# Kernel optimization log

Measured on AMD Instinct MI355X. Metric: run time of the kernel, lower is better.

## Reference

```python
import jax, jax.numpy as jnp
import numpy as np

PAD, BOS = 0, 1
EPS = 1e-08


def _lstm_cell(xt, h, c, wih, whh, bih, bhh):
    z = xt @ wih.T + h @ whh.T + bih + bhh
    i, f, g, o = jnp.split(z, 4, axis=-1)  # torch gate order i,f,g,o
    c = jax.nn.sigmoid(f) * c + jax.nn.sigmoid(i) * jnp.tanh(g)
    h = jax.nn.sigmoid(o) * jnp.tanh(c)
    return h, c


def _run_lstm(emb, wih, whh, bih, bhh):
    B, H = emb.shape[0], whh.shape[1]
    def step(carry, xt):
        h, c = _lstm_cell(xt, carry[0], carry[1], wih, whh, bih, bhh)
        return (h, c), h
    init = (jnp.zeros((B, H), emb.dtype), jnp.zeros((B, H), emb.dtype))
    (hT, cT), outs = jax.lax.scan(step, init, jnp.swapaxes(emb, 0, 1))
    return jnp.swapaxes(outs, 0, 1), hT, cT


def setup_inputs() -> dict:
    key = jax.random.key(0)
    V, H, B, S, T = 32000, 256, 8, 200, 51
    ks = jax.random.split(key, 24)
    def n(i, shape, s=0.02):
        return jax.random.normal(ks[i], shape, jnp.float32) * s
    x = jax.random.randint(ks[0], (B, S), 1, V)
    x = x.at[:, -1].set(V - 1)  # pins extended vocab size to 2V
    labels = jax.random.randint(ks[1], (B, T), 1, V)
    return {
        "x": x, "labels": labels, "ext_vocab_size": 2 * V,
        "emb_enc": n(2, (V, H)).at[PAD].set(0.0),
        "wih_f": n(3, (4 * H, H)), "whh_f": n(4, (4 * H, H)),
        "bih_f": jnp.zeros((4 * H,), jnp.float32), "bhh_f": jnp.zeros((4 * H,), jnp.float32),
        "wih_b": n(5, (4 * H, H)), "whh_b": n(6, (4 * H, H)),
        "bih_b": jnp.zeros((4 * H,), jnp.float32), "bhh_b": jnp.zeros((4 * H,), jnp.float32),
        "w_sel1": n(7, (H, 2 * H)), "b_sel1": jnp.zeros((H,), jnp.float32),
        "w_sel2": n(8, (1, H)), "b_sel2": jnp.zeros((1,), jnp.float32),
        "w_rh": n(9, (H, 2 * H)), "b_rh": jnp.zeros((H,), jnp.float32),
        "w_rc": n(10, (H, 2 * H)), "b_rc": jnp.zeros((H,), jnp.float32),
        "emb_dec": n(11, (V, H)).at[PAD].set(0.0),
        "wih_d": n(12, (4 * H, 3 * H)), "whh_d": n(13, (4 * H, H)),
        "bih_d": jnp.zeros((4 * H,), jnp.float32), "bhh_d": jnp.zeros((4 * H,), jnp.float32),
        "w_attn": n(14, (H, 4 * H)), "b_attn": jnp.zeros((H,), jnp.float32),
        "w_attn_v": n(15, (1, H)),
        "w_ptr": n(16, (1, 3 * H)), "b_ptr": jnp.zeros((1,), jnp.float32),
        "w_gen": n(17, (V, H)), "b_gen": jnp.zeros((V,), jnp.float32),
        "w_cov": n(18, (H, 1)), "b_cov": jnp.zeros((H,), jnp.float32),
    }


def reference(x, labels, ext_vocab_size, emb_enc, wih_f, whh_f, bih_f, bhh_f,
              wih_b, whh_b, bih_b, bhh_b, w_sel1, b_sel1, w_sel2, b_sel2,
              w_rh, b_rh, w_rc, b_rc, emb_dec, wih_d, whh_d, bih_d, bhh_d,
              w_attn, b_attn, w_attn_v, w_ptr, b_ptr, w_gen, b_gen, w_cov, b_cov):
    B, S = x.shape
    V, H = w_gen.shape
    # ---- Encoder: BiLSTM (no padding -> packing is identity; eval -> no dropout)
    emb = emb_enc[x]  # [B,S,H]
    out_f, h_f, c_f = _run_lstm(emb, wih_f, whh_f, bih_f, bhh_f)
    out_b_r, h_b, c_b = _run_lstm(emb[:, ::-1], wih_b, whh_b, bih_b, bhh_b)
    enc_out = jnp.concatenate([out_f, out_b_r[:, ::-1]], axis=-1)  # [B,S,2H]
    copy_probs = jax.nn.sigmoid(
        (jnp.tanh(enc_out @ w_sel1.T + b_sel1) @ w_sel2.T + b_sel2)[..., 0])  # [B,S]
    # ---- bidirectional state reduction
    h0 = jax.nn.relu(jnp.concatenate([h_f, h_b], -1) @ w_rh.T + b_rh)
    c0 = jax.nn.relu(jnp.concatenate([c_f, c_b], -1) @ w_rc.T + b_rc)
    # ---- Decoder loop (teacher forcing): inputs = [BOS, labels[:,1:T-1]]
    dec_in = jnp.concatenate(
        [jnp.full((B, 1), BOS, labels.dtype), labels[:, 1:-1]], axis=1)  # [B,T-1]
    mask_cp = (copy_probs > EPS).astype(jnp.float32)
    rows = jnp.arange(B)[:, None]

    def step(carry, tok):
        h, c, cov = carry
        cov_feat = cov[..., None] * w_cov[:, 0] + b_cov  # [B,S,H]
        feats = jnp.concatenate(
            [enc_out, jnp.broadcast_to(h[:, None, :], (B, S, H)), cov_feat], axis=-1)
        e = jnp.tanh(feats @ w_attn.T + b_attn)           # [B,S,H]
        attn = jax.nn.softmax(e @ w_attn_v[0], axis=1)    # [B,S]
        attn = attn * mask_cp
        attn = attn / (attn.sum(1, keepdims=True) + 1e-10)
        cov = cov + attn
        ctx = jnp.einsum('bs,bsd->bd', attn, enc_out)     # [B,2H]
        h, c = _lstm_cell(jnp.concatenate([emb_dec[tok], ctx], -1), h, c,
                          wih_d, whh_d, bih_d, bhh_d)
        p_gen = jax.nn.sigmoid(jnp.concatenate([ctx, h], -1) @ w_ptr.T + b_ptr)  # [B,1]
        vocab_dist = jax.nn.softmax(h @ w_gen.T + b_gen, axis=-1)  # [B,V]
        dist = jnp.zeros((B, ext_vocab_size), jnp.float32)
        dist = dist.at[:, :V].set(p_gen * vocab_dist)
        dist = dist.at[rows, x].add((1.0 - p_gen) * attn)  # pointer/copy scatter-add
        return (h, c, cov), dist

    cov0 = jnp.zeros((B, S), jnp.float32)
    _, outs = jax.lax.scan(step, (h0, c0, cov0), dec_in.T)
    outputs = jnp.swapaxes(outs, 0, 1)  # [B,T-1,EV]
    # ---- loss (faithful: CE treats the mixture distribution as logits)
    targets = labels[:, 1:]
    logp = jax.nn.log_softmax(outputs, axis=-1)
    nll = -jnp.take_along_axis(logp, targets[..., None], axis=-1)[..., 0]
    valid = (targets != PAD).astype(jnp.float32)
    loss_ce = (nll * valid).sum() / valid.sum()
    m = (x != PAD).astype(jnp.float32)
    lp = jnp.clip(jnp.log(copy_probs), -100.0, None)
    l1p = jnp.clip(jnp.log1p(-copy_probs), -100.0, None)
    bce = -(m * lp + (1.0 - m) * l1p)
    loss = loss_ce + 1.0 * (bce * m).sum() / m.sum()
    return outputs, loss
```

## Files before the change

### kernel.cpp

```cpp
#include <hip/hip_runtime.h>
#include <hip/hip_bf16.h>
#include <stdint.h>


#define DEVI __device__ __forceinline__
#define AT_RLX __ATOMIC_RELAXED
#define SC_AGT __HIP_MEMORY_SCOPE_AGENT

static constexpr size_t OFF_ACC   = 0;
static constexpr size_t OFF_FLAGE = 4;
static constexpr size_t OFF_FLAGD = 36;
static constexpr size_t ZERO_FLOATS = 200;
static constexpr size_t OFF_CTX   = 256;
static constexpr size_t OFF_EMB   = 4352;
static constexpr size_t OFF_HSEL  = OFF_EMB;
static constexpr size_t OFF_HP    = OFF_EMB;
static constexpr size_t OFF_PREF  = OFF_EMB  + 409600;
static constexpr size_t OFF_PREB  = OFF_PREF + 1638400;
static constexpr size_t OFF_BIAS  = OFF_PREB + 1638400;
static constexpr size_t OFF_HB    = OFF_BIAS + 3072;
static constexpr size_t OFF_HFIN  = OFF_HB   + 8192;
static constexpr size_t OFF_CFIN  = OFF_HFIN + 4096;
static constexpr size_t OFF_ENCOUT= OFF_CFIN + 4096;
static constexpr size_t OFF_MASK  = OFF_ENCOUT + 819200;
static constexpr size_t OFF_C0    = OFF_MASK + 1600;
static constexpr size_t OFF_EP    = OFF_C0   + 2048;
static constexpr size_t OFF_WCP   = OFF_EP   + 409600;
static constexpr size_t OFF_BCP   = OFF_WCP  + 256;
static constexpr size_t OFF_DEMB  = OFF_BCP  + 256;
static constexpr size_t OFF_DPRE  = OFF_DEMB + 102400;
static constexpr size_t OFF_HBUF  = OFF_DPRE + 409600;
static constexpr size_t OFF_CS    = OFF_HBUF + 4096;
static constexpr size_t OFF_HS    = OFF_CS   + 204800;
static constexpr size_t OFF_AS    = OFF_HS   + 102400;
static constexpr size_t OFF_PG    = OFF_AS   + 80000;
static constexpr size_t OFF_PE    = OFF_PG   + 512;

DEVI float sigf(float x)      { return 1.0f / (1.0f + __expf(-x)); }
DEVI float tanh_fast(float x) { return 1.0f - 2.0f / (1.0f + __expf(2.0f * x)); }
DEVI float ald(const float* p)  { return __hip_atomic_load((float*)p, AT_RLX, SC_AGT); }
DEVI void  ast(float* p, float v){ __hip_atomic_store(p, v, AT_RLX, SC_AGT); }

DEVI void fbar(int* flags, int g, int n, int val) {
  __syncthreads();
  if ((int)threadIdx.x == 0)
    __hip_atomic_store(flags + g, val, AT_RLX, SC_AGT);
  if ((int)threadIdx.x < n && (int)threadIdx.x != g) {
    while (__hip_atomic_load(flags + threadIdx.x, AT_RLX, SC_AGT) < val)
      __builtin_amdgcn_s_sleep(1);
  }
  __syncthreads();
}

__global__ __launch_bounds__(256) void k_biassum(
    const float* bih_f, const float* bhh_f, const float* bih_b, const float* bhh_b,
    const float* bih_d, const float* bhh_d, float* ws) {
  int i = blockIdx.x * 256 + threadIdx.x;
  int which = i >> 10, jj = i & 1023;
  float v = (which == 0) ? bih_f[jj] + bhh_f[jj]
          : (which == 1) ? bih_b[jj] + bhh_b[jj]
                         : bih_d[jj] + bhh_d[jj];
  ws[OFF_BIAS + i] = v;
}

__global__ __launch_bounds__(256) void k_embed(
    const int* xin, const int* labels, const float* emb_enc, const float* emb_dec, float* ws) {
  int r = blockIdx.x, h = threadIdx.x;
  if (r < 1600) {
    int t = r >> 3, b = r & 7;
    ws[OFF_EMB + (size_t)r * 256 + h] = emb_enc[(size_t)xin[b * 200 + t] * 256 + h];
  } else {
    int r2 = r - 1600;
    int t = r2 >> 3, b = r2 & 7;
    int tok = (t == 0) ? 1 : labels[b * 51 + t];
    ws[OFF_DEMB + (size_t)r2 * 256 + h] = emb_dec[(size_t)tok * 256 + h];
  }
}

template<int BM, int BN, int TM, int TN, int CMAP, int ACT, int AMAP>
__global__ __launch_bounds__(256) void k_gemm(
    const float* __restrict__ A, const float* __restrict__ B,
    const float* __restrict__ bias, float* __restrict__ C,
    int M, int K, int ldb, int ldc) {
  __shared__ float As[16][BM];
  __shared__ float Bs[16][BN];
  const int tid = threadIdx.x;
  const int tx = tid & 15, ty = tid >> 4;
  const int m0 = blockIdx.x * BM, n0 = blockIdx.y * BN;
  float acc[TM][TN];
#pragma unroll
  for (int i = 0; i < TM; ++i)
#pragma unroll
    for (int q = 0; q < TN; ++q) acc[i][q] = 0.f;

  for (int kk = 0; kk < K; kk += 16) {
#pragma unroll
    for (int e = tid; e < BM * 4; e += 256) {
      int m = e >> 2, k4 = (e & 3) * 4;
      int gm0 = m0 + m;
      float4 v = {0.f, 0.f, 0.f, 0.f};
      if (gm0 < M) {
        int gm = AMAP ? (((199 - (gm0 >> 3)) << 3) + (gm0 & 7)) : gm0;
        v = *(const float4*)(A + (size_t)gm * K + kk + k4);
      }
      As[k4 + 0][m] = v.x; As[k4 + 1][m] = v.y; As[k4 + 2][m] = v.z; As[k4 + 3][m] = v.w;
    }
#pragma unroll
    for (int e = tid; e < BN * 4; e += 256) {
      int n = e >> 2, k4 = (e & 3) * 4;
      float4 v = *(const float4*)(B + (size_t)(n0 + n) * ldb + kk + k4);
      Bs[k4 + 0][n] = v.x; Bs[k4 + 1][n] = v.y; Bs[k4 + 2][n] = v.z; Bs[k4 + 3][n] = v.w;
    }
    __syncthreads();
#pragma unroll
    for (int k = 0; k < 16; ++k) {
      float a[TM], bv[TN];
#pragma unroll
      for (int i = 0; i < TM; ++i) a[i] = As[k][ty * TM + i];
#pragma unroll
      for (int q = 0; q < TN; ++q) bv[q] = Bs[k][tx * TN + q];
#pragma unroll
      for (int i = 0; i < TM; ++i)
#pragma unroll
        for (int q = 0; q < TN; ++q) acc[i][q] += a[i] * bv[q];
    }
    __syncthreads();
  }
#pragma unroll
  for (int i = 0; i < TM; ++i) {
    int gm = m0 + ty * TM + i;
    if (gm >= M) continue;
    size_t base;
    if (CMAP == 1) { int t = gm >> 3, b = gm & 7; base = (size_t)(b * 50 + t) * 64000; }
    else            base = (size_t)gm * ldc;
#pragma unroll
    for (int q = 0; q < TN; ++q) {
      int n = n0 + tx * TN + q;
      float v = acc[i][q] + bias[n];
      if (ACT == 1) v = tanh_fast(v);
      C[base + n] = v;
    }
  }
}

__global__ __launch_bounds__(512, 1) void k_encoder(
    const float* __restrict__ whh_f, const float* __restrict__ whh_b, float* __restrict__ ws) {
  __shared__ float hs2[2048];
  __shared__ float zs[512];
  const int dir = blockIdx.x >> 4;
  const int p   = blockIdx.x & 15;
  const int u0  = p * 16;
  const float* whh = dir ? whh_b : whh_f;
  const float* pre = ws + (dir ? OFF_PREB : OFF_PREF);
  unsigned long long* hp = (unsigned long long*)(ws + OFF_HP);
  const int tid = threadIdx.x;
  const int kc4 = tid & 15;
  const int jp  = tid >> 4;
  const int jj0 = jp * 2, jj1 = jj0 + 1;
  const int jg0 = (jj0 >> 4) * 256 + u0 + (jj0 & 15);
  const int jg1 = (jj1 >> 4) * 256 + u0 + (jj1 & 15);
  float4 W0[4], W1[4];
  {
    const float* w0 = whh + (size_t)jg0 * 256 + kc4 * 16;
    const float* w1 = whh + (size_t)jg1 * 256 + kc4 * 16;
#pragma unroll
    for (int q = 0; q < 4; ++q) { W0[q] = *(const float4*)(w0 + q * 4);
                                  W1[q] = *(const float4*)(w1 + q * 4); }
  }
  const int jlf = kc4 >> 3, bf = kc4 & 7;
  const int jjf = jp * 2 + jlf;
  const int jf  = (jjf >> 4) * 256 + u0 + (jjf & 15);
  const int zsl = (jjf >> 4) * 128 + (jjf & 15) * 8 + bf;
  const int wb_ = tid >> 6;
  const int kk0 = (tid * 4) & 255;
  const int wdst = wb_ * 256 + ((kk0 >> 2) & 3) * 64 + (kk0 >> 4) * 4;
  const int ui2 = tid & 15, b2 = tid >> 4;
  float c_reg = 0.f;
  float* enc = ws + OFF_ENCOUT;

  for (int t = 0; t < 200; ++t) {
    float pre_v = pre[((size_t)t * 8 + bf) * 1024 + jf];
    float acc[16];
#pragma unroll
    for (int i = 0; i < 16; ++i) acc[i] = 0.f;
    if (t > 0) {
      unsigned long long* src = hp + (size_t)((((t + 1) & 1) * 2 + dir) * 2048) + tid * 4;
      const unsigned long long e = (unsigned long long)(unsigned)t;
      unsigned long long a0, a1, a2, a3;
      for (;;) {
        a0 = __hip_atomic_load(src + 0, AT_RLX, SC_AGT);
        a1 = __hip_atomic_load(src + 1, AT_RLX, SC_AGT);
        a2 = __hip_atomic_load(src + 2, AT_RLX, SC_AGT);
        a3 = __hip_atomic_load(src + 3, AT_RLX, SC_AGT);
        if (((a0 >> 32) == e) && ((a1 >> 32) == e) &&
            ((a2 >> 32) == e) && ((a3 >> 32) == e)) break;
        __builtin_amdgcn_s_sleep(1);
      }
      float4 hv;
      hv.x = __uint_as_float((unsigned)a0);
      hv.y = __uint_as_float((unsigned)a1);
      hv.z = __uint_as_float((unsigned)a2);
      hv.w = __uint_as_float((unsigned)a3);
      *(float4*)(&hs2[wdst]) = hv;
    }
    __syncthreads();
    if (t > 0) {
#pragma unroll
      for (int b = 0; b < 8; ++b) {
        const float* hb = &hs2[b * 256 + kc4 * 4];
#pragma unroll
        for (int q = 0; q < 4; ++q) {
          float4 h4 = *(const float4*)(hb + q * 64);
          acc[b]     = fmaf(W0[q].x, h4.x, acc[b]);
          acc[b]     = fmaf(W0[q].y, h4.y, acc[b]);
          acc[b]     = fmaf(W0[q].z, h4.z, acc[b]);
          acc[b]     = fmaf(W0[q].w, h4.w, acc[b]);
          acc[8 + b] = fmaf(W1[q].x, h4.x, acc[8 + b]);
          acc[8 + b] = fmaf(W1[q].y, h4.y, acc[8 + b]);
          acc[8 + b] = fmaf(W1[q].z, h4.z, acc[8 + b]);
          acc[8 + b] = fmaf(W1[q].w, h4.w, acc[8 + b]);
        }
      }
    }
    {
      bool h8 = (kc4 & 8) != 0;
#pragma unroll
      for (int i = 0; i < 8; ++i) {
        float send = h8 ? acc[i] : acc[i + 8];
        float keep = h8 ? acc[i + 8] : acc[i];
        acc[i] = keep + __shfl_xor(send, 8);
      }
      bool h4b = (kc4 & 4) != 0;
#pragma unroll
      for (int i = 0; i < 4; ++i) {
        float send = h4b ? acc[i] : acc[i + 4];
        float keep = h4b ? acc[i + 4] : acc[i];
        acc[i] = keep + __shfl_xor(send, 4);
      }
      bool h2b = (kc4 & 2) != 0;
#pragma unroll
      for (int i = 0; i < 2; ++i) {
        float send = h2b ? acc[i] : acc[i + 2];
        float keep = h2b ? acc[i + 2] : acc[i];
        acc[i] = keep + __shfl_xor(send, 2);
      }
      bool h1b = (kc4 & 1) != 0;
      {
        float send = h1b ? acc[0] : acc[1];
        float keep = h1b ? acc[1] : acc[0];
        acc[0] = keep + __shfl_xor(send, 1);
      }
    }
    zs[zsl] = acc[0] + pre_v;
    __syncthreads();
    if (tid < 128) {
      int i0 = ui2 * 8 + b2;
      float zi = zs[i0], zf = zs[128 + i0], zg = zs[256 + i0], zo = zs[384 + i0];
      float cn = sigf(zf) * c_reg + sigf(zi) * tanh_fast(zg);
      float hn = sigf(zo) * tanh_fast(cn);
      c_reg = cn;
      int uu = u0 + ui2;
      if (t < 199) {
        unsigned long long pk =
            ((unsigned long long)(unsigned)(t + 1) << 32) |
            (unsigned long long)__float_as_uint(hn);
        __hip_atomic_store(hp + (size_t)(((t & 1) * 2 + dir) * 2048) + b2 * 256 + uu,
                           pk, AT_RLX, SC_AGT);
      }
      int s = dir ? (199 - t) : t;
      enc[((size_t)b2 * 200 + s) * 512 + dir * 256 + uu] = hn;
      if (t == 199) {
        ws[OFF_HFIN + (size_t)(dir * 8 + b2) * 256 + uu] = hn;
        ws[OFF_CFIN + (size_t)(dir * 8 + b2) * 256 + uu] = cn;
      }
    }
  }
}

__global__ __launch_bounds__(64) void k_selbce(
    const float* w_sel2, const float* b_sel2, const int* xin, float* ws) {
  int r = blockIdx.x, lane = threadIdx.x;
  float pacc = 0.f;
#pragma unroll
  for (int i = 0; i < 4; ++i) {
    int k = lane + 64 * i;
    pacc += ws[OFF_HSEL + (size_t)r * 256 + k] * w_sel2[k];
  }
#pragma unroll
  for (int m = 1; m < 64; m <<= 1) pacc += __shfl_xor(pacc, m);
  if (lane == 0) {
    float cp = sigf(pacc + b_sel2[0]);
    ws[OFF_MASK + r] = (cp > 1e-8f) ? 1.f : 0.f;
    int b = r / 200, s = r % 200;
    float m = (xin[b * 200 + s] != 0) ? 1.f : 0.f;
    if (m > 0.f) {
      float lp = fmaxf(logf(cp), -100.f);
      atomicAdd(ws + OFF_ACC + 2, -lp);
    }
    atomicAdd(ws + OFF_ACC + 3, m);
  }
}

__global__ __launch_bounds__(256) void k_wcp(
    const float* w_attn, const float* w_cov, const float* b_cov, float* ws) {
  int jj = threadIdx.x;
  float a = 0.f, c = 0.f;
  for (int h = 0; h < 256; ++h) {
    float w = w_attn[(size_t)jj * 1024 + 768 + h];
    a += w * w_cov[h];
    c += w * b_cov[h];
  }
  ws[OFF_WCP + jj] = a;
  ws[OFF_BCP + jj] = c;
}

__global__ __launch_bounds__(256) void k_h0c0(
    const float* w_rh, const float* b_rh, const float* w_rc, const float* b_rc, float* ws) {
  int b = blockIdx.x, jj = threadIdx.x;
  const float* hf  = ws + OFF_HFIN + (size_t)b * 256;
  const float* hbk = ws + OFF_HFIN + 2048 + (size_t)b * 256;
  const float* cf  = ws + OFF_CFIN + (size_t)b * 256;
  const float* cbk = ws + OFF_CFIN + 2048 + (size_t)b * 256;
  float ah = b_rh[jj], ac = b_rc[jj];
  for (int k = 0; k < 256; ++k) {
    ah += hf[k] * w_rh[(size_t)jj * 512 + k];
    ac += cf[k] * w_rc[(size_t)jj * 512 + k];
  }
  for (int k = 0; k < 256; ++k) {
    ah += hbk[k] * w_rh[(size_t)jj * 512 + 256 + k];
    ac += cbk[k] * w_rc[(size_t)jj * 512 + 256 + k];
  }
  ws[OFF_C0 + (size_t)b * 256 + jj] = fmaxf(ac, 0.f);
  ws[OFF_HBUF + (size_t)b * 256 + jj] = fmaxf(ah, 0.f);
}

__global__ __launch_bounds__(512, 1) void k_decoder(
    const float* __restrict__ wih_d, const float* __restrict__ whh_d,
    const float* __restrict__ w_attn, const float* __restrict__ w_attn_v,
    float* __restrict__ ws) {
  __shared__ float hc_s[8 * 768];
  __shared__ float h_pad[264];
  __shared__ float hw_q[64];
  __shared__ float e_s[256];
  __shared__ float at_s[256], cv_s[256], msk_s[256];
  __shared__ float zs_l[256];
  __shared__ float wcq_s[64], bcq_s[64], wvq_s[64];
  __shared__ float mS_s[2];
  const int g = blockIdx.x, tid = threadIdx.x;
  const int b1 = g >> 2, sq = g & 3, s0 = sq * 50;
  int* flags = (int*)(ws + OFF_FLAGD);
  const int jl = tid >> 3, kq = tid & 7;
  const int kseg = tid & 15, row_l = tid >> 4;
  const int u_l = row_l & 7, gate = row_l >> 3;
  const int j = gate * 256 + g * 8 + u_l;
  float4 W48[12];
#pragma unroll
  for (int q = 0; q < 12; ++q) {
    int k0 = 4 * kseg + 64 * q;
    W48[q] = (k0 < 512) ? *(const float4*)(wih_d + (size_t)j * 768 + 256 + k0)
                        : *(const float4*)(whh_d + (size_t)j * 256 + (k0 - 512));
  }
  float4 W32[8];
  {
    const float* wsrc = w_attn + (size_t)(sq * 64 + jl) * 1024 + 512 + kq * 32;
#pragma unroll
    for (int q = 0; q < 8; ++q) W32[q] = *(const float4*)(wsrc + q * 4);
  }
  const int u_c = tid & 7, b_c = tid >> 3;
  float c_reg = (tid < 64) ? ws[OFF_C0 + (size_t)b_c * 256 + g * 8 + u_c] : 0.f;
  for (int s = tid; s < 256; s += 512) {
    msk_s[s] = (s < 200) ? ws[OFF_MASK + b1 * 200 + s] : 0.f;
    cv_s[s] = 0.f;
  }
  if (tid < 64) {
    wcq_s[tid] = ws[OFF_WCP + sq * 64 + tid];
    bcq_s[tid] = ws[OFF_BCP + sq * 64 + tid];
    wvq_s[tid] = w_attn_v[sq * 64 + tid];
  }
  __syncthreads();

  for (int t = 0; t < 50; ++t) {
    const int rb = t & 1, wb = 1 - rb;
    if (tid < 128) ast(ws + OFF_CTX + g * 128 + tid, 0.f);
    if (tid < 256) {
      float v = ald(ws + OFF_HBUF + (size_t)rb * 2048 + b1 * 256 + tid);
      h_pad[(tid >> 5) * 33 + (tid & 31)] = v;
    }
    __syncthreads();
    {
      float a = 0.f;
      const float* hq = &h_pad[kq * 33];
#pragma unroll
      for (int q = 0; q < 8; ++q) {
        float4 h4 = { hq[q * 4 + 0], hq[q * 4 + 1], hq[q * 4 + 2], hq[q * 4 + 3] };
        a = fmaf(W32[q].x, h4.x, a);
        a = fmaf(W32[q].y, h4.y, a);
        a = fmaf(W32[q].z, h4.z, a);
        a = fmaf(W32[q].w, h4.w, a);
      }
      a += __shfl_xor(a, 1);
      a += __shfl_xor(a, 2);
      a += __shfl_xor(a, 4);
      if (kq == 0) hw_q[jl] = a;
    }
    __syncthreads();
    if (tid < 200) {
      const int s = tid;
      float cv = cv_s[s];
      const float* ep = ws + OFF_EP + ((size_t)(b1 * 200 + s)) * 256 + sq * 64;
      float pe = 0.f;
#pragma unroll
      for (int i4 = 0; i4 < 16; ++i4) {
        float4 e4 = *(const float4*)(ep + i4 * 4);
        float4 h4 = *(const float4*)(&hw_q[i4 * 4]);
        float4 w4 = *(const float4*)(&wcq_s[i4 * 4]);
        float4 b4 = *(const float4*)(&bcq_s[i4 * 4]);
        float4 v4 = *(const float4*)(&wvq_s[i4 * 4]);
        pe = fmaf(tanh_fast(e4.x + h4.x + cv * w4.x + b4.x), v4.x, pe);
        pe = fmaf(tanh_fast(e4.y + h4.y + cv * w4.y + b4.y), v4.y, pe);
        pe = fmaf(tanh_fast(e4.z + h4.z + cv * w4.z + b4.z), v4.z, pe);
        pe = fmaf(tanh_fast(e4.w + h4.w + cv * w4.w + b4.w), v4.w, pe);
      }
      ast(ws + OFF_PE + (size_t)(sq * 8 + b1) * 200 + s, pe);
    }
    fbar(flags, g, 32, 3 * t + 1);

    if (tid < 200) {
      float e0 = ald(ws + OFF_PE + (size_t)(0 * 8 + b1) * 200 + tid);
      float e1 = ald(ws + OFF_PE + (size_t)(1 * 8 + b1) * 200 + tid);
      float e2 = ald(ws + OFF_PE + (size_t)(2 * 8 + b1) * 200 + tid);
      float e3 = ald(ws + OFF_PE + (size_t)(3 * 8 + b1) * 200 + tid);
      e_s[tid] = (e0 + e1) + (e2 + e3);
    }
    __syncthreads();
    if (tid < 64) {
      float m = -1e30f;
#pragma unroll
      for (int i = 0; i < 4; ++i) {
        int s = tid + 64 * i;
        if (s < 200) m = fmaxf(m, e_s[s]);
      }
#pragma unroll
      for (int md = 1; md < 64; md <<= 1) m = fmaxf(m, __shfl_xor(m, md));
      float es = 0.f, ems = 0.f;
#pragma unroll
      for (int i = 0; i < 4; ++i) {
        int s = tid + 64 * i;
        if (s < 200) {
          float e = __expf(e_s[s] - m);
          es += e; ems += e * msk_s[s];
        }
      }
#pragma unroll
      for (int md = 1; md < 64; md <<= 1) { es += __shfl_xor(es, md); ems += __shfl_xor(ems, md); }
      if (tid == 0) { mS_s[0] = m; mS_s[1] = 1.0f / (ems + 1e-10f * es); }
    }
    __syncthreads();
    if (tid < 200) {
      float a = __expf(e_s[tid] - mS_s[0]) * msk_s[tid] * mS_s[1];
      at_s[tid] = a;
      cv_s[tid] += a;
      if (tid >= s0 && tid < s0 + 50)
        ws[OFF_AS + ((size_t)t * 8 + b1) * 200 + tid] = a;
    }
    __syncthreads();
    {
      float ca = 0.f;
      const float* ebase = ws + OFF_ENCOUT + ((size_t)(b1 * 200 + s0)) * 512 + tid;
#pragma unroll 10
      for (int s2 = 0; s2 < 50; ++s2)
        ca = fmaf(at_s[s0 + s2], ebase[(size_t)s2 * 512], ca);
      atomicAdd(ws + OFF_CTX + b1 * 512 + tid, ca);
    }
    fbar(flags, g, 32, 3 * t + 2);

    for (int e = tid; e < 6144; e += 512) {
      int bb = e / 768, kk2 = e % 768;
      hc_s[e] = (kk2 < 512) ? ald(ws + OFF_CTX + bb * 512 + kk2)
                            : ald(ws + OFF_HBUF + (size_t)rb * 2048 + bb * 256 + (kk2 - 512));
    }
    __syncthreads();
    if (g < 8) ws[OFF_CS + ((size_t)t * 8 + g) * 512 + tid] = hc_s[g * 768 + tid];
    float acc[8];
#pragma unroll
    for (int b = 0; b < 8; ++b) acc[b] = 0.f;
#pragma unroll
    for (int q = 0; q < 12; ++q) {
      int k0 = 4 * kseg + 64 * q;
#pragma unroll
      for (int b = 0; b < 8; ++b) {
        float4 h4 = *(const float4*)(&hc_s[b * 768 + k0]);
        acc[b] = fmaf(W48[q].x, h4.x, acc[b]);
        acc[b] = fmaf(W48[q].y, h4.y, acc[b]);
        acc[b] = fmaf(W48[q].z, h4.z, acc[b]);
        acc[b] = fmaf(W48[q].w, h4.w, acc[b]);
      }
    }
    {
      bool h8 = (kseg & 8) != 0;
#pragma unroll
      for (int i = 0; i < 4; ++i) {
        float send = h8 ? acc[i] : acc[i + 4];
        float keep = h8 ? acc[i + 4] : acc[i];
        acc[i] = keep + __shfl_xor(send, 8);
      }
      bool h4b = (kseg & 4) != 0;
#pragma unroll
      for (int i = 0; i < 2; ++i) {
        float send = h4b ? acc[i] : acc[i + 2];
        float keep = h4b ? acc[i + 2] : acc[i];
        acc[i] = keep + __shfl_xor(send, 4);
      }
      bool h2b = (kseg & 2) != 0;
      {
        float send = h2b ? acc[0] : acc[1];
        float keep = h2b ? acc[1] : acc[0];
        acc[0] = keep + __shfl_xor(send, 2);
      }
      acc[0] += __shfl_xor(acc[0], 1);
    }
    {
      int bz = kseg >> 1;
      float z = acc[0] + ws[OFF_DPRE + ((size_t)t * 8 + bz) * 1024 + j];
      if ((kseg & 1) == 0) zs_l[row_l * 8 + bz] = z;
    }
    __syncthreads();
    if (tid < 64) {
      float zi = zs_l[(0  + u_c) * 8 + b_c];
      float zf = zs_l[(8  + u_c) * 8 + b_c];
      float zg = zs_l[(16 + u_c) * 8 + b_c];
      float zo = zs_l[(24 + u_c) * 8 + b_c];
      float cn = sigf(zf) * c_reg + sigf(zi) * tanh_fast(zg);
      float hn = sigf(zo) * tanh_fast(cn);
      c_reg = cn;
      ast(ws + OFF_HBUF + (size_t)wb * 2048 + b_c * 256 + g * 8 + u_c, hn);
      ws[OFF_HS + ((size_t)t * 8 + b_c) * 256 + g * 8 + u_c] = hn;
    }
    fbar(flags, g, 32, 3 * t + 3);
  }
}

__global__ __launch_bounds__(64) void k_pgen(const float* w_ptr, const float* b_ptr, float* ws) {
  int r = blockIdx.x, lane = threadIdx.x;
  float p = 0.f;
#pragma unroll
  for (int i = 0; i < 12; ++i) {
    int k = lane + 64 * i;
    float v = (k < 512) ? ws[OFF_CS + (size_t)r * 512 + k]
                        : ws[OFF_HS + (size_t)r * 256 + (k - 512)];
    p += v * w_ptr[k];
  }
#pragma unroll
  for (int m = 1; m < 64; m <<= 1) p += __shfl_xor(p, m);
  if (lane == 0) ws[OFF_PG + r] = sigf(p + b_ptr[0]);
}

__global__ __launch_bounds__(256) void k_v2(const int* xin, const int* labels, float* ws, float* out) {
  __shared__ float redm[256], reds[256];
  __shared__ int xv[200];
  __shared__ float s1sh, corrsh;
  int r = blockIdx.x, tid = threadIdx.x;
  int tt = r >> 3, b = r & 7;
  float* row = out + (size_t)(b * 50 + tt) * 64000;
  for (int i = tid; i < 200; i += 256) xv[i] = xin[b * 200 + i];
  float m = -1e30f, s = 0.f;
  for (int i = tid; i < 32000; i += 256) {
    float z = row[i];
    float nm = fmaxf(m, z);
    s = s * __expf(m - nm) + __expf(z - nm);
    m = nm;
  }
  redm[tid] = m; reds[tid] = s;
  __syncthreads();
  for (int st = 128; st >= 1; st >>= 1) {
    if (tid < st) {
      float m2 = redm[tid + st], s2 = reds[tid + st];
      float M = fmaxf(redm[tid], m2);
      reds[tid] = reds[tid] * __expf(redm[tid] - M) + s2 * __expf(m2 - M);
      redm[tid] = M;
    }
    __syncthreads();
  }
  float mx = redm[0], sum = reds[0];
  float pg = ws[OFF_PG + r];
  __syncthreads();
  float s1 = 0.f;
  float inv = 1.0f / sum;
  for (int i = tid; i < 32000; i += 256) {
    float z = row[i];
    float d = pg * (__expf(z - mx) * inv);
    row[i] = d;
    s1 += __expf(d);
  }
  for (int i = 32000 + tid; i < 64000; i += 256) row[i] = 0.0f;
  reds[tid] = s1;
  __syncthreads();
  for (int st = 128; st >= 1; st >>= 1) { if (tid < st) reds[tid] += reds[tid + st]; __syncthreads(); }
  if (tid == 0) { s1sh = reds[0]; corrsh = 0.f; }
  __syncthreads();
  if (tid < 200) {
    int v = xv[tid];
    bool own = true;
    for (int s2 = 0; s2 < tid; ++s2) if (xv[s2] == v) { own = false; break; }
    if (own) {
      float delta = 0.f;
      for (int s2 = tid; s2 < 200; ++s2)
        if (xv[s2] == v) delta += ws[OFF_AS + (size_t)r * 200 + s2];
      delta *= (1.0f - pg);
      float base = row[v];
      row[v] = base + delta;
      atomicAdd(&corrsh, __expf(base + delta) - __expf(base));
    }
  }
  __syncthreads();
  if (tid == 0) {
    float lse = logf(s1sh + corrsh + 32000.0f);
    int tgt = labels[b * 51 + tt + 1];
    float dt = row[tgt];
    float valid = (tgt != 0) ? 1.f : 0.f;
    atomicAdd(ws + OFF_ACC + 0, valid * (lse - dt));
    atomicAdd(ws + OFF_ACC + 1, valid);
  }
}

__global__ void k_loss(float* ws, float* out, int out_size) {
  out[out_size - 1] = ws[OFF_ACC + 0] / ws[OFF_ACC + 1] + ws[OFF_ACC + 2] / ws[OFF_ACC + 3];
}

extern "C" void kernel_launch(void* const* d_in, const int* in_sizes, int n_in,
                              void* d_out, int out_size, void* d_ws, size_t ws_size,
                              hipStream_t stream) {
  (void)in_sizes; (void)n_in; (void)ws_size;
  const int*   x       = (const int*)  d_in[0];
  const int*   labels  = (const int*)  d_in[1];
  const float* emb_enc = (const float*)d_in[3];
  const float* wih_f   = (const float*)d_in[4];
  const float* whh_f   = (const float*)d_in[5];
  const float* bih_f   = (const float*)d_in[6];
  const float* bhh_f   = (const float*)d_in[7];
  const float* wih_b   = (const float*)d_in[8];
  const float* whh_b   = (const float*)d_in[9];
  const float* bih_b   = (const float*)d_in[10];
  const float* bhh_b   = (const float*)d_in[11];
  const float* w_sel1  = (const float*)d_in[12];
  const float* b_sel1  = (const float*)d_in[13];
  const float* w_sel2  = (const float*)d_in[14];
  const float* b_sel2  = (const float*)d_in[15];
  const float* w_rh    = (const float*)d_in[16];
  const float* b_rh    = (const float*)d_in[17];
  const float* w_rc    = (const float*)d_in[18];
  const float* b_rc    = (const float*)d_in[19];
  const float* emb_dec = (const float*)d_in[20];
  const float* wih_d   = (const float*)d_in[21];
  const float* whh_d   = (const float*)d_in[22];
  const float* bih_d   = (const float*)d_in[23];
  const float* bhh_d   = (const float*)d_in[24];
  const float* w_attn  = (const float*)d_in[25];
  const float* b_attn  = (const float*)d_in[26];
  const float* w_attn_v= (const float*)d_in[27];
  const float* w_ptr   = (const float*)d_in[28];
  const float* b_ptr   = (const float*)d_in[29];
  const float* w_gen   = (const float*)d_in[30];
  const float* b_gen   = (const float*)d_in[31];
  const float* w_cov   = (const float*)d_in[32];
  const float* b_cov   = (const float*)d_in[33];
  float* ws  = (float*)d_ws;
  float* out = (float*)d_out;

  hipMemsetAsync(d_ws, 0, ZERO_FLOATS * 4, stream);
  k_biassum<<<12, 256, 0, stream>>>(bih_f, bhh_f, bih_b, bhh_b, bih_d, bhh_d, ws);
  k_embed<<<2000, 256, 0, stream>>>(x, labels, emb_enc, emb_dec, ws);
  k_gemm<64,64,4,4,0,0,0><<<dim3(25,16), 256, 0, stream>>>(ws+OFF_EMB,  wih_f, ws+OFF_BIAS,      ws+OFF_PREF, 1600, 256, 256, 1024);
  k_gemm<64,64,4,4,0,0,1><<<dim3(25,16), 256, 0, stream>>>(ws+OFF_EMB,  wih_b, ws+OFF_BIAS+1024, ws+OFF_PREB, 1600, 256, 256, 1024);
  k_gemm<64,64,4,4,0,0,0><<<dim3(7,16),  256, 0, stream>>>(ws+OFF_DEMB, wih_d, ws+OFF_BIAS+2048, ws+OFF_DPRE, 400,  256, 768, 1024);
  hipMemsetAsync((void*)(ws + OFF_HP), 0, (size_t)2 * 2 * 2048 * sizeof(unsigned long long), stream);
  k_encoder<<<32, 512, 0, stream>>>(whh_f, whh_b, ws);
  k_gemm<64,64,4,4,0,1,0><<<dim3(25,4),  256, 0, stream>>>(ws+OFF_ENCOUT, w_sel1, b_sel1, ws+OFF_HSEL, 1600, 512, 512, 256);
  k_selbce<<<1600, 64, 0, stream>>>(w_sel2, b_sel2, x, ws);
  k_gemm<64,64,4,4,0,0,0><<<dim3(25,4),  256, 0, stream>>>(ws+OFF_ENCOUT, w_attn, b_attn, ws+OFF_EP, 1600, 512, 1024, 256);
  k_wcp<<<1, 256, 0, stream>>>(w_attn, w_cov, b_cov, ws);
  k_h0c0<<<8, 256, 0, stream>>>(w_rh, b_rh, w_rc, b_rc, ws);
  k_decoder<<<32, 512, 0, stream>>>(wih_d, whh_d, w_attn, w_attn_v, ws);
  k_pgen<<<400, 64, 0, stream>>>(w_ptr, b_ptr, ws);
  k_gemm<128,128,8,8,1,0,0><<<dim3(4,250), 256, 0, stream>>>(ws+OFF_HS, w_gen, b_gen, out, 400, 256, 256, 64000);
  k_v2<<<400, 256, 0, stream>>>(x, labels, ws, out);
  k_loss<<<1, 1, 0, stream>>>(ws, out, out_size);
}
```

Baseline: 2.073 ms.

## Replace decoder flag barriers with step-tagged dataflow exchanges

Removes the three per-step global flag barriers in the persistent decoder kernel. Hidden state, partial attention energies and partial context vectors now travel as 64-bit words that pack the step number with the value, and consumers spin until their tag matches. The context atomicAdd becomes four per-quarter partials summed by the reader. This lets blocks proceed as soon as their own inputs are ready instead of waiting on all 32 blocks, at the cost of more polling loads, double-width traffic and an extra memset to clear the tags.

```diff
diff --git a/kernel.cpp b/kernel.cpp
--- a/kernel.cpp
+++ b/kernel.cpp
@@ -15,6 +15,10 @@
 static constexpr size_t OFF_EMB   = 4352;
 static constexpr size_t OFF_HSEL  = OFF_EMB;
 static constexpr size_t OFF_HP    = OFF_EMB;
+static constexpr size_t OFF_DHP   = OFF_EMB;
+static constexpr size_t OFF_DPE   = OFF_EMB + 8192;
+static constexpr size_t OFF_DCX   = OFF_EMB + 20992;
+static constexpr size_t DTAG_FLOATS = 53760;
 static constexpr size_t OFF_PREF  = OFF_EMB  + 409600;
 static constexpr size_t OFF_PREB  = OFF_PREF + 1638400;
 static constexpr size_t OFF_BIAS  = OFF_PREB + 1638400;
@@ -40,16 +44,11 @@
 DEVI float tanh_fast(float x) { return 1.0f - 2.0f / (1.0f + __expf(2.0f * x)); }
 DEVI float ald(const float* p)  { return __hip_atomic_load((float*)p, AT_RLX, SC_AGT); }
 DEVI void  ast(float* p, float v){ __hip_atomic_store(p, v, AT_RLX, SC_AGT); }
-
-DEVI void fbar(int* flags, int g, int n, int val) {
-  __syncthreads();
-  if ((int)threadIdx.x == 0)
-    __hip_atomic_store(flags + g, val, AT_RLX, SC_AGT);
-  if ((int)threadIdx.x < n && (int)threadIdx.x != g) {
-    while (__hip_atomic_load(flags + threadIdx.x, AT_RLX, SC_AGT) < val)
-      __builtin_amdgcn_s_sleep(1);
-  }
-  __syncthreads();
+DEVI unsigned long long aldu(const unsigned long long* p) {
+  return __hip_atomic_load((unsigned long long*)p, AT_RLX, SC_AGT);
+}
+DEVI void astu(unsigned long long* p, unsigned long long v) {
+  __hip_atomic_store(p, v, AT_RLX, SC_AGT);
 }
 
 __global__ __launch_bounds__(256) void k_biassum(
@@ -188,10 +187,7 @@
       const unsigned long long e = (unsigned long long)(unsigned)t;
       unsigned long long a0, a1, a2, a3;
       for (;;) {
-        a0 = __hip_atomic_load(src + 0, AT_RLX, SC_AGT);
-        a1 = __hip_atomic_load(src + 1, AT_RLX, SC_AGT);
-        a2 = __hip_atomic_load(src + 2, AT_RLX, SC_AGT);
-        a3 = __hip_atomic_load(src + 3, AT_RLX, SC_AGT);
+        a0 = aldu(src + 0); a1 = aldu(src + 1); a2 = aldu(src + 2); a3 = aldu(src + 3);
         if (((a0 >> 32) == e) && ((a1 >> 32) == e) &&
             ((a2 >> 32) == e) && ((a3 >> 32) == e)) break;
         __builtin_amdgcn_s_sleep(1);
@@ -264,8 +260,7 @@
         unsigned long long pk =
             ((unsigned long long)(unsigned)(t + 1) << 32) |
             (unsigned long long)__float_as_uint(hn);
-        __hip_atomic_store(hp + (size_t)(((t & 1) * 2 + dir) * 2048) + b2 * 256 + uu,
-                           pk, AT_RLX, SC_AGT);
+        astu(hp + (size_t)(((t & 1) * 2 + dir) * 2048) + b2 * 256 + uu, pk);
       }
       int s = dir ? (199 - t) : t;
       enc[((size_t)b2 * 200 + s) * 512 + dir * 256 + uu] = hn;
@@ -331,7 +326,8 @@
     ac += cbk[k] * w_rc[(size_t)jj * 512 + 256 + k];
   }
   ws[OFF_C0 + (size_t)b * 256 + jj] = fmaxf(ac, 0.f);
-  ws[OFF_HBUF + (size_t)b * 256 + jj] = fmaxf(ah, 0.f);
+  unsigned long long* hp2 = (unsigned long long*)(ws + OFF_DHP);
+  hp2[(size_t)b * 256 + jj] = (unsigned long long)__float_as_uint(fmaxf(ah, 0.f));
 }
 
 __global__ __launch_bounds__(512, 1) void k_decoder(
@@ -348,7 +344,9 @@
   __shared__ float mS_s[2];
   const int g = blockIdx.x, tid = threadIdx.x;
   const int b1 = g >> 2, sq = g & 3, s0 = sq * 50;
-  int* flags = (int*)(ws + OFF_FLAGD);
+  unsigned long long* hp2 = (unsigned long long*)(ws + OFF_DHP);
+  unsigned long long* pe2 = (unsigned long long*)(ws + OFF_DPE);
+  unsigned long long* cx2 = (unsigned long long*)(ws + OFF_DCX);
   const int jl = tid >> 3, kq = tid & 7;
   const int kseg = tid & 15, row_l = tid >> 4;
   const int u_l = row_l & 7, gate = row_l >> 3;
@@ -381,10 +379,17 @@
 
   for (int t = 0; t < 50; ++t) {
     const int rb = t & 1, wb = 1 - rb;
-    if (tid < 128) ast(ws + OFF_CTX + g * 128 + tid, 0.f);
+    const unsigned long long tgH = (unsigned long long)(unsigned)t;
+    const unsigned long long tgP = (unsigned long long)(unsigned)(t + 1);
     if (tid < 256) {
-      float v = ald(ws + OFF_HBUF + (size_t)rb * 2048 + b1 * 256 + tid);
-      h_pad[(tid >> 5) * 33 + (tid & 31)] = v;
+      unsigned long long* src = hp2 + (size_t)rb * 2048 + b1 * 256 + tid;
+      unsigned long long v;
+      for (;;) {
+        v = aldu(src);
+        if ((v >> 32) == tgH) break;
+        __builtin_amdgcn_s_sleep(1);
+      }
+      h_pad[(tid >> 5) * 33 + (tid & 31)] = __uint_as_float((unsigned)v);
     }
     __syncthreads();
     {
@@ -421,16 +426,24 @@
         pe = fmaf(tanh_fast(e4.z + h4.z + cv * w4.z + b4.z), v4.z, pe);
         pe = fmaf(tanh_fast(e4.w + h4.w + cv * w4.w + b4.w), v4.w, pe);
       }
-      ast(ws + OFF_PE + (size_t)(sq * 8 + b1) * 200 + s, pe);
-    }
-    fbar(flags, g, 32, 3 * t + 1);
+      astu(pe2 + (size_t)(sq * 8 + b1) * 200 + s,
+           (tgP << 32) | (unsigned long long)__float_as_uint(pe));
+    }
 
     if (tid < 200) {
-      float e0 = ald(ws + OFF_PE + (size_t)(0 * 8 + b1) * 200 + tid);
-      float e1 = ald(ws + OFF_PE + (size_t)(1 * 8 + b1) * 200 + tid);
-      float e2 = ald(ws + OFF_PE + (size_t)(2 * 8 + b1) * 200 + tid);
-      float e3 = ald(ws + OFF_PE + (size_t)(3 * 8 + b1) * 200 + tid);
-      e_s[tid] = (e0 + e1) + (e2 + e3);
+      float esum = 0.f;
+#pragma unroll
+      for (int q = 0; q < 4; ++q) {
+        unsigned long long* src = pe2 + (size_t)(q * 8 + b1) * 200 + tid;
+        unsigned long long v;
+        for (;;) {
+          v = aldu(src);
+          if ((v >> 32) == tgP) break;
+          __builtin_amdgcn_s_sleep(1);
+        }
+        esum += __uint_as_float((unsigned)v);
+      }
+      e_s[tid] = esum;
     }
     __syncthreads();
     if (tid < 64) {
@@ -470,14 +483,38 @@
 #pragma unroll 10
       for (int s2 = 0; s2 < 50; ++s2)
         ca = fmaf(at_s[s0 + s2], ebase[(size_t)s2 * 512], ca);
-      atomicAdd(ws + OFF_CTX + b1 * 512 + tid, ca);
-    }
-    fbar(flags, g, 32, 3 * t + 2);
+      astu(cx2 + (size_t)(sq * 8 + b1) * 512 + tid,
+           (tgP << 32) | (unsigned long long)__float_as_uint(ca));
+    }
 
     for (int e = tid; e < 6144; e += 512) {
       int bb = e / 768, kk2 = e % 768;
-      hc_s[e] = (kk2 < 512) ? ald(ws + OFF_CTX + bb * 512 + kk2)
-                            : ald(ws + OFF_HBUF + (size_t)rb * 2048 + bb * 256 + (kk2 - 512));
+      float val;
+      if (kk2 < 512) {
+        unsigned long long* p0 = cx2 + (size_t)(0 * 8 + bb) * 512 + kk2;
+        unsigned long long* p1 = cx2 + (size_t)(1 * 8 + bb) * 512 + kk2;
+        unsigned long long* p2 = cx2 + (size_t)(2 * 8 + bb) * 512 + kk2;
+        unsigned long long* p3 = cx2 + (size_t)(3 * 8 + bb) * 512 + kk2;
+        unsigned long long v0, v1, v2, v3;
+        for (;;) {
+          v0 = aldu(p0); v1 = aldu(p1); v2 = aldu(p2); v3 = aldu(p3);
+          if (((v0 >> 32) == tgP) && ((v1 >> 32) == tgP) &&
+              ((v2 >> 32) == tgP) && ((v3 >> 32) == tgP)) break;
+          __builtin_amdgcn_s_sleep(1);
+        }
+        val = (__uint_as_float((unsigned)v0) + __uint_as_float((unsigned)v1)) +
+              (__uint_as_float((unsigned)v2) + __uint_as_float((unsigned)v3));
+      } else {
+        unsigned long long* src = hp2 + (size_t)rb * 2048 + bb * 256 + (kk2 - 512);
+        unsigned long long v;
+        for (;;) {
+          v = aldu(src);
+          if ((v >> 32) == tgH) break;
+          __builtin_amdgcn_s_sleep(1);
+        }
+        val = __uint_as_float((unsigned)v);
+      }
+      hc_s[e] = val;
     }
     __syncthreads();
     if (g < 8) ws[OFF_CS + ((size_t)t * 8 + g) * 512 + tid] = hc_s[g * 768 + tid];
@@ -533,10 +570,10 @@
       float cn = sigf(zf) * c_reg + sigf(zi) * tanh_fast(zg);
       float hn = sigf(zo) * tanh_fast(cn);
       c_reg = cn;
-      ast(ws + OFF_HBUF + (size_t)wb * 2048 + b_c * 256 + g * 8 + u_c, hn);
+      astu(hp2 + (size_t)wb * 2048 + b_c * 256 + g * 8 + u_c,
+           (tgP << 32) | (unsigned long long)__float_as_uint(hn));
       ws[OFF_HS + ((size_t)t * 8 + b_c) * 256 + g * 8 + u_c] = hn;
     }
-    fbar(flags, g, 32, 3 * t + 3);
   }
 }
 
@@ -677,6 +714,7 @@
   k_encoder<<<32, 512, 0, stream>>>(whh_f, whh_b, ws);
   k_gemm<64,64,4,4,0,1,0><<<dim3(25,4),  256, 0, stream>>>(ws+OFF_ENCOUT, w_sel1, b_sel1, ws+OFF_HSEL, 1600, 512, 512, 256);
   k_selbce<<<1600, 64, 0, stream>>>(w_sel2, b_sel2, x, ws);
+  hipMemsetAsync((void*)(ws + OFF_EMB), 0, DTAG_FLOATS * sizeof(float), stream);
   k_gemm<64,64,4,4,0,0,0><<<dim3(25,4),  256, 0, stream>>>(ws+OFF_ENCOUT, w_attn, b_attn, ws+OFF_EP, 1600, 512, 1024, 256);
   k_wcp<<<1, 256, 0, stream>>>(w_attn, w_cov, b_cov, ws);
   k_h0c0<<<8, 256, 0, stream>>>(w_rh, b_rh, w_rc, b_rc, ws);
```

New measurement: 2.140 ms. +3.2%, slower.

## Retile decoder gate matvec so each thread computes four rows over wider k-segments

Applied to the files above, without the earlier changes.

The decoder LSTM gate matvec is remapped so each wavefront covers all 768 k values and each thread holds weights for four gate rows. Every float4 of h/ctx read from LDS is reused across four rows, which cuts LDS traffic per FMA. The LDS staging layout is permuted to match, and the CS write is folded into the staging loop. In exchange the accumulator array grows from 8 to 32, adding register pressure, and the cross-lane reduction gets longer.

```diff
diff --git a/kernel.cpp b/kernel.cpp
--- a/kernel.cpp
+++ b/kernel.cpp
@@ -40,6 +40,12 @@
 DEVI float tanh_fast(float x) { return 1.0f - 2.0f / (1.0f + __expf(2.0f * x)); }
 DEVI float ald(const float* p)  { return __hip_atomic_load((float*)p, AT_RLX, SC_AGT); }
 DEVI void  ast(float* p, float v){ __hip_atomic_store(p, v, AT_RLX, SC_AGT); }
+DEVI unsigned long long aldu(const unsigned long long* p) {
+  return __hip_atomic_load((unsigned long long*)p, AT_RLX, SC_AGT);
+}
+DEVI void astu(unsigned long long* p, unsigned long long v) {
+  __hip_atomic_store(p, v, AT_RLX, SC_AGT);
+}
 
 DEVI void fbar(int* flags, int g, int n, int val) {
   __syncthreads();
@@ -188,10 +194,7 @@
       const unsigned long long e = (unsigned long long)(unsigned)t;
       unsigned long long a0, a1, a2, a3;
       for (;;) {
-        a0 = __hip_atomic_load(src + 0, AT_RLX, SC_AGT);
-        a1 = __hip_atomic_load(src + 1, AT_RLX, SC_AGT);
-        a2 = __hip_atomic_load(src + 2, AT_RLX, SC_AGT);
-        a3 = __hip_atomic_load(src + 3, AT_RLX, SC_AGT);
+        a0 = aldu(src + 0); a1 = aldu(src + 1); a2 = aldu(src + 2); a3 = aldu(src + 3);
         if (((a0 >> 32) == e) && ((a1 >> 32) == e) &&
             ((a2 >> 32) == e) && ((a3 >> 32) == e)) break;
         __builtin_amdgcn_s_sleep(1);
@@ -264,8 +267,7 @@
         unsigned long long pk =
             ((unsigned long long)(unsigned)(t + 1) << 32) |
             (unsigned long long)__float_as_uint(hn);
-        __hip_atomic_store(hp + (size_t)(((t & 1) * 2 + dir) * 2048) + b2 * 256 + uu,
-                           pk, AT_RLX, SC_AGT);
+        astu(hp + (size_t)(((t & 1) * 2 + dir) * 2048) + b2 * 256 + uu, pk);
       }
       int s = dir ? (199 - t) : t;
       enc[((size_t)b2 * 200 + s) * 512 + dir * 256 + uu] = hn;
@@ -350,16 +352,24 @@
   const int b1 = g >> 2, sq = g & 3, s0 = sq * 50;
   int* flags = (int*)(ws + OFF_FLAGD);
   const int jl = tid >> 3, kq = tid & 7;
-  const int kseg = tid & 15, row_l = tid >> 4;
-  const int u_l = row_l & 7, gate = row_l >> 3;
-  const int j = gate * 256 + g * 8 + u_l;
-  float4 W48[12];
-#pragma unroll
-  for (int q = 0; q < 12; ++q) {
-    int k0 = 4 * kseg + 64 * q;
-    W48[q] = (k0 < 512) ? *(const float4*)(wih_d + (size_t)j * 768 + 256 + k0)
-                        : *(const float4*)(whh_d + (size_t)j * 256 + (k0 - 512));
-  }
+  const int ks = tid & 63;
+  const int rq = tid >> 6;
+  float4 W[12];
+#pragma unroll
+  for (int rl = 0; rl < 4; ++rl) {
+    int row = rq * 4 + rl;
+    int jrow = (row >> 3) * 256 + g * 8 + (row & 7);
+#pragma unroll
+    for (int q = 0; q < 3; ++q) {
+      int k0 = ks * 12 + q * 4;
+      W[rl * 3 + q] = (k0 < 512)
+          ? *(const float4*)(wih_d + (size_t)jrow * 768 + 256 + k0)
+          : *(const float4*)(whh_d + (size_t)jrow * 256 + (k0 - 512));
+    }
+  }
+  const int rowo = rq * 4 + ((tid >> 3) & 3);
+  const int bo   = tid & 7;
+  const int jo   = (rowo >> 3) * 256 + g * 8 + (rowo & 7);
   float4 W32[8];
   {
     const float* wsrc = w_attn + (size_t)(sq * 64 + jl) * 1024 + 512 + kq * 32;
@@ -476,53 +486,73 @@
 
     for (int e = tid; e < 6144; e += 512) {
       int bb = e / 768, kk2 = e % 768;
-      hc_s[e] = (kk2 < 512) ? ald(ws + OFF_CTX + bb * 512 + kk2)
-                            : ald(ws + OFF_HBUF + (size_t)rb * 2048 + bb * 256 + (kk2 - 512));
-    }
-    __syncthreads();
-    if (g < 8) ws[OFF_CS + ((size_t)t * 8 + g) * 512 + tid] = hc_s[g * 768 + tid];
-    float acc[8];
-#pragma unroll
-    for (int b = 0; b < 8; ++b) acc[b] = 0.f;
-#pragma unroll
-    for (int q = 0; q < 12; ++q) {
-      int k0 = 4 * kseg + 64 * q;
+      float val = (kk2 < 512) ? ald(ws + OFF_CTX + bb * 512 + kk2)
+                              : ald(ws + OFF_HBUF + (size_t)rb * 2048 + bb * 256 + (kk2 - 512));
+      int sseg = kk2 / 12, srem = kk2 % 12;
+      hc_s[bb * 768 + (srem >> 2) * 256 + sseg * 4 + (srem & 3)] = val;
+      if (g < 8 && bb == g && kk2 < 512)
+        ws[OFF_CS + ((size_t)t * 8 + g) * 512 + kk2] = val;
+    }
+    __syncthreads();
+    float acc[32];
+#pragma unroll
+    for (int i = 0; i < 32; ++i) acc[i] = 0.f;
+#pragma unroll
+    for (int q = 0; q < 3; ++q) {
+      const int kof = q * 256 + ks * 4;
 #pragma unroll
       for (int b = 0; b < 8; ++b) {
-        float4 h4 = *(const float4*)(&hc_s[b * 768 + k0]);
-        acc[b] = fmaf(W48[q].x, h4.x, acc[b]);
-        acc[b] = fmaf(W48[q].y, h4.y, acc[b]);
-        acc[b] = fmaf(W48[q].z, h4.z, acc[b]);
-        acc[b] = fmaf(W48[q].w, h4.w, acc[b]);
+        float4 h4 = *(const float4*)(&hc_s[b * 768 + kof]);
+#pragma unroll
+        for (int rl = 0; rl < 4; ++rl) {
+          float4 w4 = W[rl * 3 + q];
+          acc[rl * 8 + b] = fmaf(w4.x, h4.x, acc[rl * 8 + b]);
+          acc[rl * 8 + b] = fmaf(w4.y, h4.y, acc[rl * 8 + b]);
+          acc[rl * 8 + b] = fmaf(w4.z, h4.z, acc[rl * 8 + b]);
+          acc[rl * 8 + b] = fmaf(w4.w, h4.w, acc[rl * 8 + b]);
+        }
       }
     }
     {
-      bool h8 = (kseg & 8) != 0;
+      bool s16 = (ks & 16) != 0;
+#pragma unroll
+      for (int i = 0; i < 16; ++i) {
+        float send = s16 ? acc[i] : acc[i + 16];
+        float keep = s16 ? acc[i + 16] : acc[i];
+        acc[i] = keep + __shfl_xor(send, 16);
+      }
+      bool s8 = (ks & 8) != 0;
+#pragma unroll
+      for (int i = 0; i < 8; ++i) {
+        float send = s8 ? acc[i] : acc[i + 8];
+        float keep = s8 ? acc[i + 8] : acc[i];
+        acc[i] = keep + __shfl_xor(send, 8);
+      }
+      bool s4 = (ks & 4) != 0;
 #pragma unroll
       for (int i = 0; i < 4; ++i) {
-        float send = h8 ? acc[i] : acc[i + 4];
-        float keep = h8 ? acc[i + 4] : acc[i];
-        acc[i] = keep + __shfl_xor(send, 8);
-      }
-      bool h4b = (kseg & 4) != 0;
+        float send = s4 ? acc[i] : acc[i + 4];
+        float keep = s4 ? acc[i + 4] : acc[i];
+        acc[i] = keep + __shfl_xor(send, 4);
+      }
+      bool s2 = (ks & 2) != 0;
 #pragma unroll
       for (int i = 0; i < 2; ++i) {
-        float send = h4b ? acc[i] : acc[i + 2];
-        float keep = h4b ? acc[i + 2] : acc[i];
-        acc[i] = keep + __shfl_xor(send, 4);
-      }
-      bool h2b = (kseg & 2) != 0;
+        float send = s2 ? acc[i] : acc[i + 2];
+        float keep = s2 ? acc[i + 2] : acc[i];
+        acc[i] = keep + __shfl_xor(send, 2);
+      }
+      bool s1 = (ks & 1) != 0;
       {
-        float send = h2b ? acc[0] : acc[1];
-        float keep = h2b ? acc[1] : acc[0];
-        acc[0] = keep + __shfl_xor(send, 2);
-      }
-      acc[0] += __shfl_xor(acc[0], 1);
+        float send = s1 ? acc[0] : acc[1];
+        float keep = s1 ? acc[1] : acc[0];
+        acc[0] = keep + __shfl_xor(send, 1);
+      }
+      acc[0] += __shfl_xor(acc[0], 32);
     }
     {
-      int bz = kseg >> 1;
-      float z = acc[0] + ws[OFF_DPRE + ((size_t)t * 8 + bz) * 1024 + j];
-      if ((kseg & 1) == 0) zs_l[row_l * 8 + bz] = z;
+      float z = acc[0] + ws[OFF_DPRE + ((size_t)t * 8 + bo) * 1024 + jo];
+      if ((tid & 32) == 0) zs_l[rowo * 8 + bo] = z;
     }
     __syncthreads();
     if (tid < 64) {
```

Measured after the change: 2.110 ms. No clear change (+1.8%).
